# Kernel tuning notes

Measured on AMD Instinct MI355X. Metric: run time of the kernel, lower is better.

The kernel has to match this reference:

```python
import jax, jax.numpy as jnp
import numpy as np

H, VS, VT, S, T = 512, 32000, 32000, 256, 256
EPS = 1e-12


def _normalize(x):
    # torch.nn.functional.normalize over last dim, p=2, eps=1e-12
    n = jnp.sqrt(jnp.sum(x * x, axis=-1, keepdims=True))
    return x / jnp.maximum(n, EPS)


def setup_inputs() -> dict:
    key = jax.random.key(0)
    ks = jax.random.split(key, 16)
    std = 0.01
    return {
        'src_nums': jax.random.randint(ks[0], (S,), 0, VS, dtype=jnp.int32),
        'tgt_nums': jax.random.randint(ks[1], (T,), 0, VT, dtype=jnp.int32),
        'enc_emb_W': std * jax.random.normal(ks[2], (VS, H), jnp.float32),
        'enc_h0': std * jax.random.normal(ks[3], (H,), jnp.float32),
        'enc_W_hi': std * jax.random.normal(ks[4], (H, H), jnp.float32),
        'enc_W_hh': std * jax.random.normal(ks[5], (H, H), jnp.float32),
        'enc_b': std * jax.random.normal(ks[6], (H,), jnp.float32),
        'dec_emb_W': std * jax.random.normal(ks[7], (VT, H), jnp.float32),
        'dec_h0': std * jax.random.normal(ks[8], (H,), jnp.float32),
        'dec_W_hi': std * jax.random.normal(ks[9], (H, H), jnp.float32),
        'dec_W_hh': std * jax.random.normal(ks[10], (H, H), jnp.float32),
        'dec_b': std * jax.random.normal(ks[11], (H,), jnp.float32),
        'tnh_W': std * jax.random.normal(ks[12], (H, 2 * H), jnp.float32),
        'tnh_b': std * jax.random.normal(ks[13], (H,), jnp.float32),
        'out_W': std * jax.random.normal(ks[14], (VT, H), jnp.float32),
    }


def reference(src_nums, tgt_nums, enc_emb_W, enc_h0, enc_W_hi, enc_W_hh, enc_b,
              dec_emb_W, dec_h0, dec_W_hi, dec_W_hh, dec_b, tnh_W, tnh_b, out_W):
    # ---- Encoder: embed + normalize, then sequential RNN ----
    src_emb = _normalize(enc_emb_W[src_nums])  # [S, H]

    def enc_step(h, e):
        h2 = jnp.tanh(enc_W_hi @ e + enc_W_hh @ h + enc_b)
        return h2, h2

    _, hs = jax.lax.scan(enc_step, enc_h0, src_emb)
    h_seq = jnp.concatenate([enc_h0[None, :], hs], axis=0)  # [S+1, H]

    # ---- Decoder: per-step attention + output + teacher-forced input ----
    def dec_step(h, t):
        # Bahdanau-style dot attention over encoder states
        weights = jax.nn.softmax(h_seq @ h)        # [S+1]
        c = weights @ h_seq                         # [H]
        z = jnp.tanh(tnh_W @ jnp.concatenate([c, h]) + tnh_b)  # [H]
        logp = jax.nn.log_softmax(out_W @ z)        # [VT]
        nll = -logp[t]
        e = _normalize(dec_emb_W[t])                # [H]
        h2 = jnp.tanh(dec_W_hi @ e + dec_W_hh @ h + dec_b)
        return h2, nll

    _, nlls = jax.lax.scan(dec_step, dec_h0, tgt_nums)
    return jnp.mean(nlls)
```

## Files before the change

kernel.cpp:

```cpp
#include <hip/hip_runtime.h>

typedef _Float16 f16;
typedef _Float16 f16x2 __attribute__((ext_vector_type(2)));
typedef _Float16 half8 __attribute__((ext_vector_type(8)));
typedef float f32x4 __attribute__((ext_vector_type(4)));

#define Hh 512
#define TT 256
#define VTOT 32000
#define S4H 100.0f

__device__ inline int dot8i4(int a, int b, int c) {
#if __has_builtin(__builtin_amdgcn_sdot8)
    return __builtin_amdgcn_sdot8(a, b, c, false);
#else
    int s = c;
#pragma unroll
    for (int i = 0; i < 8; ++i)
        s += ((a << (28 - 4 * i)) >> 28) * ((b << (28 - 4 * i)) >> 28);
    return s;
#endif
}

__device__ inline float tanh_fast(float x) {
    float ax = fabsf(x);
    float t = __expf(-2.f * ax);
    float th = (1.f - t) * __builtin_amdgcn_rcpf(1.f + t);
    return copysignf(th, x);
}

__device__ inline float block_sum(float v, float* red) {
#pragma unroll
    for (int o = 1; o < 64; o <<= 1) v += __shfl_xor(v, o);
    if ((threadIdx.x & 63) == 0) red[threadIdx.x >> 6] = v;
    __syncthreads();
    v = red[0] + red[1] + red[2] + red[3];
    __syncthreads();
    return v;
}

__device__ inline float block_max(float v, float* red) {
#pragma unroll
    for (int o = 1; o < 64; o <<= 1) v = fmaxf(v, __shfl_xor(v, o));
    if ((threadIdx.x & 63) == 0) red[threadIdx.x >> 6] = v;
    __syncthreads();
    v = fmaxf(fmaxf(red[0], red[1]), fmaxf(red[2], red[3]));
    __syncthreads();
    return v;
}

__global__ void __launch_bounds__(256) k_prep(
    const int* __restrict__ src, const int* __restrict__ tgt,
    const float* __restrict__ encW, const float* __restrict__ decW,
    const float* __restrict__ eh0, const float* __restrict__ dh0,
    const float* __restrict__ encWhh, const float* __restrict__ decWhh,
    float* __restrict__ emb, float* __restrict__ h_seq, float* __restrict__ Hd,
    unsigned int* __restrict__ Wq, float* __restrict__ sWf) {
    const int b = blockIdx.x, tid = threadIdx.x;
    if (b >= 514) {
        const int bc = b - 514;
        const int R = bc * 4 + (tid >> 6);
        const int c = R >> 9, r = R & 511, j = tid & 63;
        const float* s = (c ? decWhh : encWhh) + (size_t)r * Hh + j * 8;
        float4 v0 = ((const float4*)s)[0];
        float4 v1 = ((const float4*)s)[1];
        float vv[8] = {v0.x, v0.y, v0.z, v0.w, v1.x, v1.y, v1.z, v1.w};
        float m = 0.f;
#pragma unroll
        for (int k = 0; k < 8; ++k) m = fmaxf(m, fabsf(vv[k]));
#pragma unroll
        for (int o = 1; o < 64; o <<= 1) m = fmaxf(m, __shfl_xor(m, o));
        m = fmaxf(m, 1e-30f);
        float qs = 7.f / m;
        unsigned int dw = 0;
#pragma unroll
        for (int k = 0; k < 8; ++k) {
            int q = (int)rintf(vv[k] * qs);
            dw |= ((unsigned int)(q & 0xF)) << (4 * k);
        }
        const int u = j >> 2, dwi = j & 3;
        Wq[((((size_t)(c * 16 + u)) * 512 + r) << 2) + dwi] = dw;
        if (j == 0) sWf[c * 512 + r] = m * (1.f / (7.f * S4H));
        return;
    }
    if (b >= 512) {
        const int c = b - 512;
        float2 v = ((const float2*)(c ? dh0 : eh0))[tid];
        if (c == 0)
            ((float2*)h_seq)[tid] = v;
        else
            ((float2*)Hd)[tid] = v;
        return;
    }
    const int c = b >> 8, t = b & 255;
    const int idx = c ? tgt[t] : src[t];
    const float* row = (c ? decW : encW) + (size_t)idx * Hh;
    float2 v = ((const float2*)row)[tid];
    __shared__ float red[4];
    float tot = block_sum(v.x * v.x + v.y * v.y, red);
    float inv = 1.f / fmaxf(sqrtf(tot), 1e-12f);
    float* orow = emb + ((size_t)c * TT + t) * Hh;
    float2 o;
    o.x = v.x * inv;
    o.y = v.y * inv;
    ((float2*)orow)[tid] = o;
}

__global__ void __launch_bounds__(256) k_proj(const float* __restrict__ emb,
                                              const float* __restrict__ eWhi,
                                              const float* __restrict__ eb,
                                              const float* __restrict__ dWhi,
                                              const float* __restrict__ db,
                                              float* __restrict__ P) {
    const int c = blockIdx.y, t0 = blockIdx.x * 4, tid = threadIdx.x;
    const int i = tid + blockIdx.z * 256;
    const float* Wv = c ? dWhi : eWhi;
    const float* b = c ? db : eb;
    __shared__ __align__(16) float esh[4][Hh];
#pragma unroll
    for (int rr = 0; rr < 4; ++rr) {
        ((float2*)esh[rr])[tid] =
            ((const float2*)(emb + ((size_t)c * TT + t0 + rr) * Hh))[tid];
    }
    __syncthreads();
    const float4* wp = (const float4*)(Wv + (size_t)i * Hh);
    float acc[4] = {0.f, 0.f, 0.f, 0.f};
    for (int j = 0; j < Hh / 4; ++j) {
        float4 w0 = wp[j];
#pragma unroll
        for (int rr = 0; rr < 4; ++rr) {
            float4 e = ((const float4*)esh[rr])[j];
            acc[rr] += w0.x * e.x + w0.y * e.y + w0.z * e.z + w0.w * e.w;
        }
    }
    float b0 = b[i];
#pragma unroll
    for (int rr = 0; rr < 4; ++rr)
        P[((size_t)c * TT + t0 + rr) * Hh + i] = acc[rr] + b0;
}

__global__ void __launch_bounds__(512, 2) k_chain(
    const uint4* __restrict__ Wq, const float* __restrict__ sWf,
    const float* __restrict__ P, const float* __restrict__ eh0,
    const float* __restrict__ dh0, float* __restrict__ h_seq,
    float* __restrict__ Hd) {
    const int c = blockIdx.x, t = threadIdx.x;
    __shared__ __align__(16) int hq[2][64];

    uint4 wq[16];
#pragma unroll
    for (int u = 0; u < 16; ++u) wq[u] = Wq[(size_t)(c * 16 + u) * 512 + t];
#pragma unroll
    for (int u = 0; u < 16; ++u)
        asm volatile("" : "+v"(wq[u].x), "+v"(wq[u].y), "+v"(wq[u].z),
                          "+v"(wq[u].w));
    const float frow = sWf[c * 512 + t];

    {
        float hv = (c ? dh0 : eh0)[t];
        int q = (int)rintf(fminf(fmaxf(hv * S4H, -7.f), 7.f));
        int b1 = (q & 0xF) | ((__shfl_down(q, 1) & 0xF) << 4);
        int b2 = (b1 & 0xFF) | ((__shfl_down(b1, 2) & 0xFF) << 8);
        int b4 = (b2 & 0xFFFF) | (__shfl_down(b2, 4) << 16);
        if ((t & 7) == 0) hq[0][t >> 3] = b4;
    }
    __syncthreads();

    const float* Pc = P + (size_t)c * TT * Hh;
    float pv = Pc[t];

    for (int step = 0; step < 256; ++step) {
        float pvn;
        if (step < 255) pvn = Pc[(size_t)(step + 1) * Hh + t];
        const uint4* hp = (const uint4*)hq[step & 1];
        int a0 = 0, a1 = 0;
#pragma unroll
        for (int u = 0; u < 16; ++u) {
            uint4 hv = hp[u];
            uint4 w0 = wq[u];
            a0 = dot8i4((int)w0.x, (int)hv.x, a0);
            a1 = dot8i4((int)w0.y, (int)hv.y, a1);
            a0 = dot8i4((int)w0.z, (int)hv.z, a0);
            a1 = dot8i4((int)w0.w, (int)hv.w, a1);
        }
        float hnew = tanh_fast((float)(a0 + a1) * frow + pv);
        pv = pvn;
        if (c == 0)
            h_seq[(size_t)(step + 1) * Hh + t] = hnew;
        else if (step < 255)
            Hd[(size_t)(step + 1) * Hh + t] = hnew;
        int q = (int)rintf(fminf(fmaxf(hnew * S4H, -7.f), 7.f));
        int b1 = (q & 0xF) | ((__shfl_down(q, 1) & 0xF) << 4);
        int b2 = (b1 & 0xFF) | ((__shfl_down(b1, 2) & 0xFF) << 8);
        int b4 = (b2 & 0xFFFF) | (__shfl_down(b2, 4) << 16);
        if ((t & 7) == 0) hq[(step + 1) & 1][t >> 3] = b4;
        asm volatile("s_waitcnt lgkmcnt(0)\ns_barrier" ::: "memory");
    }
}

__global__ void __launch_bounds__(256) k_scores(const float* __restrict__ h_seq,
                                                const float* __restrict__ Hd,
                                                float* __restrict__ CH) {
    const int t = blockIdx.x, tid = threadIdx.x;
    __shared__ float h[Hh];
    __shared__ float w[257];
    __shared__ float red[4];
    ((float2*)h)[tid] = ((const float2*)(Hd + (size_t)t * Hh))[tid];
    __syncthreads();
    float sc0, sc1 = -3.0e38f;
    {
        const float4* row = (const float4*)(h_seq + (size_t)tid * Hh);
        float a = 0.f;
        for (int j = 0; j < Hh / 4; ++j) {
            float4 v = row[j];
            a += v.x * h[4 * j] + v.y * h[4 * j + 1] + v.z * h[4 * j + 2] +
                 v.w * h[4 * j + 3];
        }
        sc0 = a;
    }
    if (tid == 0) {
        const float4* row = (const float4*)(h_seq + (size_t)256 * Hh);
        float a = 0.f;
        for (int j = 0; j < Hh / 4; ++j) {
            float4 v = row[j];
            a += v.x * h[4 * j] + v.y * h[4 * j + 1] + v.z * h[4 * j + 2] +
                 v.w * h[4 * j + 3];
        }
        sc1 = a;
    }
    float m = block_max(fmaxf(sc0, sc1), red);
    float e0 = expf(sc0 - m);
    float e1 = (tid == 0) ? expf(sc1 - m) : 0.f;
    float tot = block_sum(e0 + e1, red);
    float inv = 1.f / tot;
    w[tid] = e0 * inv;
    if (tid == 0) w[256] = e1 * inv;
    __syncthreads();
    float* chrow = CH + (size_t)t * (2 * Hh);
    {
        const float2* hs2 = (const float2*)h_seq;
        float2 a = {0.f, 0.f}, a2 = {0.f, 0.f};
        for (int s = 0; s < 256; s += 2) {
            float2 v0 = hs2[(size_t)s * 256 + tid];
            float2 v1 = hs2[(size_t)(s + 1) * 256 + tid];
            a.x += w[s] * v0.x;
            a.y += w[s] * v0.y;
            a2.x += w[s + 1] * v1.x;
            a2.y += w[s + 1] * v1.y;
        }
        float2 vl = hs2[(size_t)256 * 256 + tid];
        float2 o;
        o.x = a.x + a2.x + w[256] * vl.x;
        o.y = a.y + a2.y + w[256] * vl.y;
        ((float2*)chrow)[tid] = o;
    }
    ((float2*)(chrow + Hh))[tid] = ((const float2*)h)[tid];
}

__global__ void __launch_bounds__(256) k_zgemm(const float* __restrict__ CH,
                                               const float* __restrict__ tnhW,
                                               const float* __restrict__ tnhb,
                                               f16* __restrict__ Zh) {
    const int t0 = blockIdx.x * 4, tid = threadIdx.x;
    const int i = tid + blockIdx.y * 256;
    __shared__ __align__(16) float chs[4][2 * Hh];
#pragma unroll
    for (int rr = 0; rr < 4; ++rr) {
        ((float4*)chs[rr])[tid] =
            ((const float4*)(CH + (size_t)(t0 + rr) * 2 * Hh))[tid];
    }
    __syncthreads();
    const float4* wp = (const float4*)(tnhW + (size_t)i * 2 * Hh);
    float acc[4] = {0.f, 0.f, 0.f, 0.f};
    for (int j = 0; j < 2 * Hh / 4; ++j) {
        float4 w0 = wp[j];
#pragma unroll
        for (int rr = 0; rr < 4; ++rr) {
            float4 e = ((const float4*)chs[rr])[j];
            acc[rr] += w0.x * e.x + w0.y * e.y + w0.z * e.z + w0.w * e.w;
        }
    }
    float b0 = tnhb[i];
#pragma unroll
    for (int rr = 0; rr < 4; ++rr)
        Zh[(size_t)(t0 + rr) * Hh + i] = (f16)tanhf(acc[rr] + b0);
}

__global__ void __launch_bounds__(256) k_logits(const f16* __restrict__ Zh,
                                                const float* __restrict__ outW,
                                                const int* __restrict__ tgt,
                                                float* __restrict__ denom,
                                                float* __restrict__ ltgt) {
    const int v0 = blockIdx.x * 64, tid = threadIdx.x;
    const int w = tid >> 6, l = tid & 63;
    const int l15 = l & 15, l4 = l >> 4;
    __shared__ __align__(16) f16 Wt[64][136];
    __shared__ __align__(16) f16 Zt[256][136];
    __shared__ float tsum[4][256];
    __shared__ int tgs[256];
    if (tid < 256) tgs[tid] = tgt[tid];

    f32x4 acc[16];
#pragma unroll
    for (int tt = 0; tt < 16; ++tt) acc[tt] = (f32x4){0.f, 0.f, 0.f, 0.f};

    for (int kc = 0; kc < 4; ++kc) {
        const int k0 = kc * 128;
#pragma unroll
        for (int p = 0; p < 8; ++p) {
            int g = p * 256 + tid;
            int row = g >> 5, f4 = g & 31;
            float4 v = *((const float4*)(outW + (size_t)(v0 + row) * Hh + k0 + f4 * 4));
            f16x2 lo = {(f16)v.x, (f16)v.y};
            f16x2 hi = {(f16)v.z, (f16)v.w};
            uint2 u;
            u.x = __builtin_bit_cast(unsigned, lo);
            u.y = __builtin_bit_cast(unsigned, hi);
            *((uint2*)&Wt[row][f4 * 4]) = u;
        }
#pragma unroll
        for (int p = 0; p < 16; ++p) {
            int g = p * 256 + tid;
            int row = g >> 4, u = g & 15;
            *((uint4*)&Zt[row][u * 8]) =
                *((const uint4*)(Zh + (size_t)row * Hh + k0 + u * 8));
        }
        __syncthreads();
        half8 a[4];
#pragma unroll
        for (int ks = 0; ks < 4; ++ks)
            a[ks] = *((const half8*)&Wt[w * 16 + l15][ks * 32 + l4 * 8]);
#pragma unroll
        for (int tt = 0; tt < 16; ++tt) {
#pragma unroll
            for (int ks = 0; ks < 4; ++ks) {
                half8 b = *((const half8*)&Zt[tt * 16 + l15][ks * 32 + l4 * 8]);
                acc[tt] = __builtin_amdgcn_mfma_f32_16x16x32_f16(a[ks], b, acc[tt],
                                                                 0, 0, 0);
            }
        }
        __syncthreads();
    }
    const int vbase = v0 + w * 16 + l4 * 4;
#pragma unroll
    for (int tt = 0; tt < 16; ++tt) {
        float e = __expf(acc[tt][0]) + __expf(acc[tt][1]) + __expf(acc[tt][2]) +
                  __expf(acc[tt][3]);
        e += __shfl_xor(e, 16);
        e += __shfl_xor(e, 32);
        if (l4 == 0) tsum[w][tt * 16 + l15] = e;
        int tglob = tt * 16 + l15;
        int rel = tgs[tglob] - vbase;
        if (rel >= 0 && rel < 4) {
            float val = (rel == 0) ? acc[tt][0]
                        : (rel == 1) ? acc[tt][1]
                        : (rel == 2) ? acc[tt][2]
                                     : acc[tt][3];
            ltgt[tglob] = val;
        }
    }
    __syncthreads();
    if (tid < 256) {
        float s = tsum[0][tid] + tsum[1][tid] + tsum[2][tid] + tsum[3][tid];
        atomicAdd(&denom[tid], s);
    }
}

__global__ void k_final(const float* __restrict__ denom, const float* __restrict__ ltgt,
                        float* __restrict__ out) {
    const int t = threadIdx.x;
    float nll = logf(denom[t]) - ltgt[t];
    __shared__ float red[4];
    float v = nll;
#pragma unroll
    for (int o = 1; o < 64; o <<= 1) v += __shfl_xor(v, o);
    if ((t & 63) == 0) red[t >> 6] = v;
    __syncthreads();
    if (t == 0) out[0] = (red[0] + red[1] + red[2] + red[3]) * (1.f / 256.f);
}

extern "C" void kernel_launch(void* const* d_in, const int* in_sizes, int n_in,
                              void* d_out, int out_size, void* d_ws, size_t ws_size,
                              hipStream_t stream) {
    (void)in_sizes; (void)n_in; (void)out_size; (void)ws_size;
    const int* src = (const int*)d_in[0];
    const int* tgt = (const int*)d_in[1];
    const float* enc_emb = (const float*)d_in[2];
    const float* enc_h0 = (const float*)d_in[3];
    const float* enc_Whi = (const float*)d_in[4];
    const float* enc_Whh = (const float*)d_in[5];
    const float* enc_b = (const float*)d_in[6];
    const float* dec_emb = (const float*)d_in[7];
    const float* dec_h0 = (const float*)d_in[8];
    const float* dec_Whi = (const float*)d_in[9];
    const float* dec_Whh = (const float*)d_in[10];
    const float* dec_b = (const float*)d_in[11];
    const float* tnhW = (const float*)d_in[12];
    const float* tnhb = (const float*)d_in[13];
    const float* outW = (const float*)d_in[14];
    float* out = (float*)d_out;
    char* ws = (char*)d_ws;

    float* denom = (float*)ws;
    float* ltgt = (float*)(ws + 1024);
    size_t off = 4096;
    float* emb = (float*)(ws + off);    off += (size_t)2 * TT * Hh * 4;
    float* P = (float*)(ws + off);      off += (size_t)2 * TT * Hh * 4;
    float* h_seq = (float*)(ws + off);  off += (size_t)264 * Hh * 4;
    float* Hd = (float*)(ws + off);     off += (size_t)256 * Hh * 4;
    float* CH = (float*)(ws + off);     off += (size_t)TT * 2 * Hh * 4;
    f16* Zh = (f16*)(ws + off);         off += (size_t)TT * Hh * 2;
    uint4* Wq = (uint4*)(ws + off);     off += (size_t)2 * Hh * Hh;
    float* sWf = (float*)(ws + off);    off += (size_t)2 * Hh * 4;

    hipMemsetAsync(ws, 0, 4096, stream);
    k_prep<<<770, 256, 0, stream>>>(src, tgt, enc_emb, dec_emb, enc_h0, dec_h0,
                                    enc_Whh, dec_Whh, emb, h_seq, Hd,
                                    (unsigned int*)Wq, sWf);
    k_proj<<<dim3(64, 2, 2), 256, 0, stream>>>(emb, enc_Whi, enc_b, dec_Whi, dec_b, P);
    k_chain<<<2, 512, 0, stream>>>(Wq, sWf, P, enc_h0, dec_h0, h_seq, Hd);
    k_scores<<<256, 256, 0, stream>>>(h_seq, Hd, CH);
    k_zgemm<<<dim3(64, 2), 256, 0, stream>>>(CH, tnhW, tnhb, Zh);
    k_logits<<<500, 256, 0, stream>>>(Zh, outW, tgt, denom, ltgt);
    k_final<<<1, 256, 0, stream>>>(denom, ltgt, out);
}
```

Before: 308.1 us.

## Use fp16 MFMA for input projection and batch two steps per attention block

The per-step input projection GEMM now runs on fp16 MFMA tiles, with normalized embeddings stored in fp16 and weights converted while loading into shared memory. The attention scoring kernel handles two decoder steps per block so each h_seq read is shared between them. The tanh projection GEMM processes eight rows per block instead of four to reuse weight loads more. This cuts redundant global reads and scalar FMA work at the cost of fp16 rounding in the projection and fewer blocks in flight for the smaller kernels.

```diff
diff --git a/kernel.cpp b/kernel.cpp
--- a/kernel.cpp
+++ b/kernel.cpp
@@ -54,7 +54,7 @@
     const float* __restrict__ encW, const float* __restrict__ decW,
     const float* __restrict__ eh0, const float* __restrict__ dh0,
     const float* __restrict__ encWhh, const float* __restrict__ decWhh,
-    float* __restrict__ emb, float* __restrict__ h_seq, float* __restrict__ Hd,
+    f16* __restrict__ embH, float* __restrict__ h_seq, float* __restrict__ Hd,
     unsigned int* __restrict__ Wq, float* __restrict__ sWf) {
     const int b = blockIdx.x, tid = threadIdx.x;
     if (b >= 514) {
@@ -99,44 +99,81 @@
     __shared__ float red[4];
     float tot = block_sum(v.x * v.x + v.y * v.y, red);
     float inv = 1.f / fmaxf(sqrtf(tot), 1e-12f);
-    float* orow = emb + ((size_t)c * TT + t) * Hh;
-    float2 o;
-    o.x = v.x * inv;
-    o.y = v.y * inv;
-    ((float2*)orow)[tid] = o;
-}
-
-__global__ void __launch_bounds__(256) k_proj(const float* __restrict__ emb,
-                                              const float* __restrict__ eWhi,
-                                              const float* __restrict__ eb,
-                                              const float* __restrict__ dWhi,
-                                              const float* __restrict__ db,
-                                              float* __restrict__ P) {
-    const int c = blockIdx.y, t0 = blockIdx.x * 4, tid = threadIdx.x;
-    const int i = tid + blockIdx.z * 256;
+    f16* orow = embH + ((size_t)c * TT + t) * Hh;
+    f16x2 o = {(f16)(v.x * inv), (f16)(v.y * inv)};
+    ((f16x2*)orow)[tid] = o;
+}
+
+__global__ void __launch_bounds__(256) k_pgemm(const f16* __restrict__ embH,
+                                               const float* __restrict__ eWhi,
+                                               const float* __restrict__ eb,
+                                               const float* __restrict__ dWhi,
+                                               const float* __restrict__ db,
+                                               float* __restrict__ P) {
+    const int c = blockIdx.y;
+    const int v0 = blockIdx.x * 64, tid = threadIdx.x;
     const float* Wv = c ? dWhi : eWhi;
-    const float* b = c ? db : eb;
-    __shared__ __align__(16) float esh[4][Hh];
-#pragma unroll
-    for (int rr = 0; rr < 4; ++rr) {
-        ((float2*)esh[rr])[tid] =
-            ((const float2*)(emb + ((size_t)c * TT + t0 + rr) * Hh))[tid];
-    }
-    __syncthreads();
-    const float4* wp = (const float4*)(Wv + (size_t)i * Hh);
-    float acc[4] = {0.f, 0.f, 0.f, 0.f};
-    for (int j = 0; j < Hh / 4; ++j) {
-        float4 w0 = wp[j];
-#pragma unroll
-        for (int rr = 0; rr < 4; ++rr) {
-            float4 e = ((const float4*)esh[rr])[j];
-            acc[rr] += w0.x * e.x + w0.y * e.y + w0.z * e.z + w0.w * e.w;
-        }
-    }
-    float b0 = b[i];
-#pragma unroll
-    for (int rr = 0; rr < 4; ++rr)
-        P[((size_t)c * TT + t0 + rr) * Hh + i] = acc[rr] + b0;
+    const float* bias = c ? db : eb;
+    const f16* Zb = embH + (size_t)c * TT * Hh;
+    const int w = tid >> 6, l = tid & 63;
+    const int l15 = l & 15, l4 = l >> 4;
+    __shared__ __align__(16) f16 Wt[64][136];
+    __shared__ __align__(16) f16 Zt[256][136];
+
+    f32x4 acc[16];
+#pragma unroll
+    for (int tt = 0; tt < 16; ++tt) acc[tt] = (f32x4){0.f, 0.f, 0.f, 0.f};
+
+    for (int kc = 0; kc < 4; ++kc) {
+        const int k0 = kc * 128;
+#pragma unroll
+        for (int p = 0; p < 8; ++p) {
+            int g = p * 256 + tid;
+            int row = g >> 5, f4 = g & 31;
+            float4 v = *((const float4*)(Wv + (size_t)(v0 + row) * Hh + k0 + f4 * 4));
+            f16x2 lo = {(f16)v.x, (f16)v.y};
+            f16x2 hi = {(f16)v.z, (f16)v.w};
+            uint2 u;
+            u.x = __builtin_bit_cast(unsigned, lo);
+            u.y = __builtin_bit_cast(unsigned, hi);
+            *((uint2*)&Wt[row][f4 * 4]) = u;
+        }
+#pragma unroll
+        for (int p = 0; p < 16; ++p) {
+            int g = p * 256 + tid;
+            int row = g >> 4, u = g & 15;
+            *((uint4*)&Zt[row][u * 8]) =
+                *((const uint4*)(Zb + (size_t)row * Hh + k0 + u * 8));
+        }
+        __syncthreads();
+        half8 a[4];
+#pragma unroll
+        for (int ks = 0; ks < 4; ++ks)
+            a[ks] = *((const half8*)&Wt[w * 16 + l15][ks * 32 + l4 * 8]);
+#pragma unroll
+        for (int tt = 0; tt < 16; ++tt) {
+#pragma unroll
+            for (int ks = 0; ks < 4; ++ks) {
+                half8 b = *((const half8*)&Zt[tt * 16 + l15][ks * 32 + l4 * 8]);
+                acc[tt] = __builtin_amdgcn_mfma_f32_16x16x32_f16(a[ks], b, acc[tt],
+                                                                 0, 0, 0);
+            }
+        }
+        __syncthreads();
+    }
+    const int ibase = v0 + w * 16 + l4 * 4;
+    float b0 = bias[ibase], b1 = bias[ibase + 1];
+    float b2 = bias[ibase + 2], b3 = bias[ibase + 3];
+#pragma unroll
+    for (int tt = 0; tt < 16; ++tt) {
+        int t = tt * 16 + l15;
+        float4 st;
+        st.x = acc[tt][0] + b0;
+        st.y = acc[tt][1] + b1;
+        st.z = acc[tt][2] + b2;
+        st.w = acc[tt][3] + b3;
+        *((float4*)(P + ((size_t)c * TT + t) * Hh + ibase)) = st;
+    }
 }
 
 __global__ void __launch_bounds__(512, 2) k_chain(
@@ -201,88 +238,97 @@
 __global__ void __launch_bounds__(256) k_scores(const float* __restrict__ h_seq,
                                                 const float* __restrict__ Hd,
                                                 float* __restrict__ CH) {
-    const int t = blockIdx.x, tid = threadIdx.x;
-    __shared__ float h[Hh];
-    __shared__ float w[257];
+    const int t0 = blockIdx.x * 2, tid = threadIdx.x;
+    __shared__ float h0s[Hh], h1s[Hh];
+    __shared__ float w0[257], w1[257];
     __shared__ float red[4];
-    ((float2*)h)[tid] = ((const float2*)(Hd + (size_t)t * Hh))[tid];
-    __syncthreads();
-    float sc0, sc1 = -3.0e38f;
+    ((float2*)h0s)[tid] = ((const float2*)(Hd + (size_t)t0 * Hh))[tid];
+    ((float2*)h1s)[tid] = ((const float2*)(Hd + (size_t)(t0 + 1) * Hh))[tid];
+    __syncthreads();
+    float a0 = 0.f, a1 = 0.f;
     {
         const float4* row = (const float4*)(h_seq + (size_t)tid * Hh);
-        float a = 0.f;
         for (int j = 0; j < Hh / 4; ++j) {
             float4 v = row[j];
-            a += v.x * h[4 * j] + v.y * h[4 * j + 1] + v.z * h[4 * j + 2] +
-                 v.w * h[4 * j + 3];
-        }
-        sc0 = a;
-    }
+            a0 += v.x * h0s[4 * j] + v.y * h0s[4 * j + 1] + v.z * h0s[4 * j + 2] +
+                  v.w * h0s[4 * j + 3];
+            a1 += v.x * h1s[4 * j] + v.y * h1s[4 * j + 1] + v.z * h1s[4 * j + 2] +
+                  v.w * h1s[4 * j + 3];
+        }
+    }
+    float sb0 = -3.0e38f, sb1 = -3.0e38f;
     if (tid == 0) {
         const float4* row = (const float4*)(h_seq + (size_t)256 * Hh);
-        float a = 0.f;
+        float x0 = 0.f, x1 = 0.f;
         for (int j = 0; j < Hh / 4; ++j) {
             float4 v = row[j];
-            a += v.x * h[4 * j] + v.y * h[4 * j + 1] + v.z * h[4 * j + 2] +
-                 v.w * h[4 * j + 3];
-        }
-        sc1 = a;
-    }
-    float m = block_max(fmaxf(sc0, sc1), red);
-    float e0 = expf(sc0 - m);
-    float e1 = (tid == 0) ? expf(sc1 - m) : 0.f;
-    float tot = block_sum(e0 + e1, red);
-    float inv = 1.f / tot;
-    w[tid] = e0 * inv;
-    if (tid == 0) w[256] = e1 * inv;
-    __syncthreads();
-    float* chrow = CH + (size_t)t * (2 * Hh);
-    {
-        const float2* hs2 = (const float2*)h_seq;
-        float2 a = {0.f, 0.f}, a2 = {0.f, 0.f};
-        for (int s = 0; s < 256; s += 2) {
-            float2 v0 = hs2[(size_t)s * 256 + tid];
-            float2 v1 = hs2[(size_t)(s + 1) * 256 + tid];
-            a.x += w[s] * v0.x;
-            a.y += w[s] * v0.y;
-            a2.x += w[s + 1] * v1.x;
-            a2.y += w[s + 1] * v1.y;
-        }
-        float2 vl = hs2[(size_t)256 * 256 + tid];
-        float2 o;
-        o.x = a.x + a2.x + w[256] * vl.x;
-        o.y = a.y + a2.y + w[256] * vl.y;
-        ((float2*)chrow)[tid] = o;
-    }
-    ((float2*)(chrow + Hh))[tid] = ((const float2*)h)[tid];
+            x0 += v.x * h0s[4 * j] + v.y * h0s[4 * j + 1] + v.z * h0s[4 * j + 2] +
+                  v.w * h0s[4 * j + 3];
+            x1 += v.x * h1s[4 * j] + v.y * h1s[4 * j + 1] + v.z * h1s[4 * j + 2] +
+                  v.w * h1s[4 * j + 3];
+        }
+        sb0 = x0;
+        sb1 = x1;
+    }
+    float m0 = block_max(fmaxf(a0, sb0), red);
+    float e0 = expf(a0 - m0);
+    float ee0 = (tid == 0) ? expf(sb0 - m0) : 0.f;
+    float tot0 = block_sum(e0 + ee0, red);
+    float inv0 = 1.f / tot0;
+    w0[tid] = e0 * inv0;
+    if (tid == 0) w0[256] = ee0 * inv0;
+    float m1 = block_max(fmaxf(a1, sb1), red);
+    float e1 = expf(a1 - m1);
+    float ee1 = (tid == 0) ? expf(sb1 - m1) : 0.f;
+    float tot1 = block_sum(e1 + ee1, red);
+    float inv1 = 1.f / tot1;
+    w1[tid] = e1 * inv1;
+    if (tid == 0) w1[256] = ee1 * inv1;
+    __syncthreads();
+    const float2* hs2 = (const float2*)h_seq;
+    float2 c0 = {0.f, 0.f}, c1 = {0.f, 0.f};
+    for (int s = 0; s < 257; ++s) {
+        float2 v = hs2[(size_t)s * 256 + tid];
+        float W0 = w0[s], W1 = w1[s];
+        c0.x += W0 * v.x;
+        c0.y += W0 * v.y;
+        c1.x += W1 * v.x;
+        c1.y += W1 * v.y;
+    }
+    float* ch0 = CH + (size_t)t0 * (2 * Hh);
+    float* ch1 = CH + (size_t)(t0 + 1) * (2 * Hh);
+    ((float2*)ch0)[tid] = c0;
+    ((float2*)ch1)[tid] = c1;
+    ((float2*)(ch0 + Hh))[tid] = ((float2*)h0s)[tid];
+    ((float2*)(ch1 + Hh))[tid] = ((float2*)h1s)[tid];
 }
 
 __global__ void __launch_bounds__(256) k_zgemm(const float* __restrict__ CH,
                                                const float* __restrict__ tnhW,
                                                const float* __restrict__ tnhb,
                                                f16* __restrict__ Zh) {
-    const int t0 = blockIdx.x * 4, tid = threadIdx.x;
+    const int t0 = blockIdx.x * 8, tid = threadIdx.x;
     const int i = tid + blockIdx.y * 256;
-    __shared__ __align__(16) float chs[4][2 * Hh];
-#pragma unroll
-    for (int rr = 0; rr < 4; ++rr) {
+    __shared__ __align__(16) float chs[8][2 * Hh];
+#pragma unroll
+    for (int rr = 0; rr < 8; ++rr) {
         ((float4*)chs[rr])[tid] =
             ((const float4*)(CH + (size_t)(t0 + rr) * 2 * Hh))[tid];
     }
     __syncthreads();
     const float4* wp = (const float4*)(tnhW + (size_t)i * 2 * Hh);
-    float acc[4] = {0.f, 0.f, 0.f, 0.f};
+    float acc[8] = {0.f, 0.f, 0.f, 0.f, 0.f, 0.f, 0.f, 0.f};
     for (int j = 0; j < 2 * Hh / 4; ++j) {
         float4 w0 = wp[j];
 #pragma unroll
-        for (int rr = 0; rr < 4; ++rr) {
+        for (int rr = 0; rr < 8; ++rr) {
             float4 e = ((const float4*)chs[rr])[j];
             acc[rr] += w0.x * e.x + w0.y * e.y + w0.z * e.z + w0.w * e.w;
         }
     }
     float b0 = tnhb[i];
 #pragma unroll
-    for (int rr = 0; rr < 4; ++rr)
+    for (int rr = 0; rr < 8; ++rr)
         Zh[(size_t)(t0 + rr) * Hh + i] = (f16)tanhf(acc[rr] + b0);
 }
 
@@ -404,7 +450,7 @@
     float* denom = (float*)ws;
     float* ltgt = (float*)(ws + 1024);
     size_t off = 4096;
-    float* emb = (float*)(ws + off);    off += (size_t)2 * TT * Hh * 4;
+    f16* embH = (f16*)(ws + off);       off += (size_t)2 * TT * Hh * 4;
     float* P = (float*)(ws + off);      off += (size_t)2 * TT * Hh * 4;
     float* h_seq = (float*)(ws + off);  off += (size_t)264 * Hh * 4;
     float* Hd = (float*)(ws + off);     off += (size_t)256 * Hh * 4;
@@ -415,12 +461,12 @@
 
     hipMemsetAsync(ws, 0, 4096, stream);
     k_prep<<<770, 256, 0, stream>>>(src, tgt, enc_emb, dec_emb, enc_h0, dec_h0,
-                                    enc_Whh, dec_Whh, emb, h_seq, Hd,
+                                    enc_Whh, dec_Whh, embH, h_seq, Hd,
                                     (unsigned int*)Wq, sWf);
-    k_proj<<<dim3(64, 2, 2), 256, 0, stream>>>(emb, enc_Whi, enc_b, dec_Whi, dec_b, P);
+    k_pgemm<<<dim3(8, 2), 256, 0, stream>>>(embH, enc_Whi, enc_b, dec_Whi, dec_b, P);
     k_chain<<<2, 512, 0, stream>>>(Wq, sWf, P, enc_h0, dec_h0, h_seq, Hd);
-    k_scores<<<256, 256, 0, stream>>>(h_seq, Hd, CH);
-    k_zgemm<<<dim3(64, 2), 256, 0, stream>>>(CH, tnhW, tnhb, Zh);
+    k_scores<<<128, 256, 0, stream>>>(h_seq, Hd, CH);
+    k_zgemm<<<dim3(32, 2), 256, 0, stream>>>(CH, tnhW, tnhb, Zh);
     k_logits<<<500, 256, 0, stream>>>(Zh, outW, tgt, denom, ltgt);
     k_final<<<1, 256, 0, stream>>>(denom, ltgt, out);
 }
```

Result: slower. 317.9 us (+3.2%).
